# Kernel tuning notes

Hardware: AMD Instinct MI355X
Metric: run time of the kernel (lower is better)

## Reference

```python
import jax, jax.numpy as jnp
import numpy as np

B, NIMG, NTXT, D, H, MLP = 2, 2048, 256, 1024, 16, 4096
DH = D // H
EPS = 1e-6

def _ln(x):
    mu = jnp.mean(x, axis=-1, keepdims=True)
    var = jnp.var(x, axis=-1, keepdims=True)
    return (x - mu) * jax.lax.rsqrt(var + EPS)

def _mod(x, shift, scale):
    return x * (1.0 + scale[:, None, :]) + shift[:, None, :]

def setup_inputs():
    key = jax.random.key(0)
    ks = jax.random.split(key, 40)
    def w(i, shape):
        return jax.random.normal(ks[i], shape, jnp.float32) * 0.02
    inp = {
        'img_tokens': jax.random.normal(ks[0], (B, NIMG, D), jnp.float32),
        'txt_tokens': jax.random.normal(ks[1], (B, NTXT, D), jnp.float32),
        'c': jax.random.normal(ks[2], (B, D), jnp.float32),
    }
    for i, n in enumerate(['q_img', 'k_img', 'v_img', 'q_txt', 'k_txt', 'v_txt', 'out_img', 'out_txt']):
        inp[n + '_w'] = w(3 + i, (D, D))
        inp[n + '_b'] = w(11 + i, (D,))
    inp['mlp_img_w1'] = w(19, (MLP, D)); inp['mlp_img_b1'] = w(20, (MLP,))
    inp['mlp_img_w2'] = w(21, (D, MLP)); inp['mlp_img_b2'] = w(22, (D,))
    inp['mlp_txt_w1'] = w(23, (MLP, D)); inp['mlp_txt_b1'] = w(24, (MLP,))
    inp['mlp_txt_w2'] = w(25, (D, MLP)); inp['mlp_txt_b2'] = w(26, (D,))
    inp['adaln_img_w'] = w(27, (6 * D, D)); inp['adaln_img_b'] = w(28, (6 * D,))
    inp['adaln_txt_w'] = w(29, (6 * D, D)); inp['adaln_txt_b'] = w(30, (6 * D,))
    return inp

def reference(img_tokens, txt_tokens, c,
              q_img_w, q_img_b, k_img_w, k_img_b, v_img_w, v_img_b,
              q_txt_w, q_txt_b, k_txt_w, k_txt_b, v_txt_w, v_txt_b,
              out_img_w, out_img_b, out_txt_w, out_txt_b,
              mlp_img_w1, mlp_img_b1, mlp_img_w2, mlp_img_b2,
              mlp_txt_w1, mlp_txt_b1, mlp_txt_w2, mlp_txt_b2,
              adaln_img_w, adaln_img_b, adaln_txt_w, adaln_txt_b):
    lin = lambda x, w, b: x @ w.T + b
    mod_i = lin(jax.nn.silu(c), adaln_img_w, adaln_img_b)
    mod_t = lin(jax.nn.silu(c), adaln_txt_w, adaln_txt_b)
    sh_a_i, sc_a_i, g_a_i, sh_m_i, sc_m_i, g_m_i = jnp.split(mod_i, 6, axis=-1)
    sh_a_t, sc_a_t, g_a_t, sh_m_t, sc_m_t, g_m_t = jnp.split(mod_t, 6, axis=-1)
    img_n = _mod(_ln(img_tokens), sh_a_i, sc_a_i)
    txt_n = _mod(_ln(txt_tokens), sh_a_t, sc_a_t)
    heads = lambda x: x.reshape(x.shape[0], x.shape[1], H, DH)  # (B, N, H, DH)
    q_i = heads(lin(img_n, q_img_w, q_img_b))
    k_i = heads(lin(img_n, k_img_w, k_img_b))
    v_i = heads(lin(img_n, v_img_w, v_img_b))
    q_t = heads(lin(txt_n, q_txt_w, q_txt_b))
    k_t = heads(lin(txt_n, k_txt_w, k_txt_b))
    v_t = heads(lin(txt_n, v_txt_w, v_txt_b))
    # joint KV: each query attends over img+txt keys
    k_j = jnp.concatenate([k_i, k_t], axis=1)  # (B, NIMG+NTXT, H, DH)
    v_j = jnp.concatenate([v_i, v_t], axis=1)
    scale = DH ** -0.5
    def attend(q):
        s = jnp.einsum('bqhd,bkhd->bhqk', q, k_j) * scale
        a = jax.nn.softmax(s, axis=-1)
        o = jnp.einsum('bhqk,bkhd->bqhd', a, v_j)
        return o.reshape(o.shape[0], o.shape[1], D)
    a_img = lin(attend(q_i), out_img_w, out_img_b)
    a_txt = lin(attend(q_t), out_txt_w, out_txt_b)
    img = img_tokens + g_a_i[:, None, :] * a_img
    txt = txt_tokens + g_a_t[:, None, :] * a_txt
    mlp = lambda x, w1, b1, w2, b2: lin(jax.nn.gelu(lin(x, w1, b1), approximate=True), w2, b2)
    img = img + g_m_i[:, None, :] * mlp(_mod(_ln(img), sh_m_i, sc_m_i), mlp_img_w1, mlp_img_b1, mlp_img_w2, mlp_img_b2)
    txt = txt + g_m_t[:, None, :] * mlp(_mod(_ln(txt), sh_m_t, sc_m_t), mlp_txt_w1, mlp_txt_b1, mlp_txt_w2, mlp_txt_b2)
    return (img, txt)
```

## Files before the change

kernel.cpp:

```cpp
#include <hip/hip_runtime.h>
#include <hip/hip_bf16.h>

typedef __bf16 bf16_t;
typedef __bf16 bf16x8 __attribute__((ext_vector_type(8)));
typedef float f32x4 __attribute__((ext_vector_type(4)));

#define DEV static __device__ __forceinline__

#define QSCALE 0.18033688011112042f

DEV float gelu_tanh(float x){
    float x3 = x*x*x;
    return 0.5f*x*(1.0f + tanhf(0.79788456080286535588f*(x + 0.044715f*x3)));
}

DEV void gload16(const void* g, void* l){
    __builtin_amdgcn_global_load_lds((const __attribute__((address_space(1))) void*)g,
                                     (__attribute__((address_space(3))) void*)l, 16, 0, 0);
}

__global__ __launch_bounds__(256) void convert_pack(
    const float* qiw, const float* kiw, const float* viw,
    const float* qtw, const float* ktw, const float* vtw,
    const float* oiw, const float* otw,
    const float* m1iw, const float* m1tw, const float* m2iw, const float* m2tw,
    const float* qib, const float* kib, const float* vib,
    const float* qtb, const float* ktb, const float* vtb,
    bf16_t* wqkvI, bf16_t* wqkvT, bf16_t* woI, bf16_t* woT,
    bf16_t* wm1I, bf16_t* wm1T, bf16_t* wm2I, bf16_t* wm2T,
    float* qkvbI, float* qkvbT)
{
    const int MB = 1048576, MB4 = 4194304;
    int seg = blockIdx.y;
    const float* src = nullptr; bf16_t* dst = nullptr; float* dstf = nullptr; int n = 0;
    switch (seg){
        case 0:  src=qiw;  dst=wqkvI;        n=MB;   break;
        case 1:  src=kiw;  dst=wqkvI+MB;     n=MB;   break;
        case 2:  src=viw;  dst=wqkvI+2*MB;   n=MB;   break;
        case 3:  src=qtw;  dst=wqkvT;        n=MB;   break;
        case 4:  src=ktw;  dst=wqkvT+MB;     n=MB;   break;
        case 5:  src=vtw;  dst=wqkvT+2*MB;   n=MB;   break;
        case 6:  src=oiw;  dst=woI;          n=MB;   break;
        case 7:  src=otw;  dst=woT;          n=MB;   break;
        case 8:  src=m1iw; dst=wm1I;         n=MB4;  break;
        case 9:  src=m1tw; dst=wm1T;         n=MB4;  break;
        case 10: src=m2iw; dst=wm2I;         n=MB4;  break;
        case 11: src=m2tw; dst=wm2T;         n=MB4;  break;
        case 12: src=qib;  dstf=qkvbI;       n=1024; break;
        case 13: src=kib;  dstf=qkvbI+1024;  n=1024; break;
        case 14: src=vib;  dstf=qkvbI+2048;  n=1024; break;
        case 15: src=qtb;  dstf=qkvbT;       n=1024; break;
        case 16: src=ktb;  dstf=qkvbT+1024;  n=1024; break;
        case 17: src=vtb;  dstf=qkvbT+2048;  n=1024; break;
    }
    float scl = (seg==0 || seg==3 || seg==12 || seg==15) ? QSCALE : 1.0f;
    int n4 = n >> 2;
    for (int i = blockIdx.x*blockDim.x + threadIdx.x; i < n4; i += gridDim.x*blockDim.x){
        float4 v = ((const float4*)src)[i];
        v.x *= scl; v.y *= scl; v.z *= scl; v.w *= scl;
        if (dst){
            union { bf16_t b[4]; uint2 q; } o;
            o.b[0] = (bf16_t)v.x; o.b[1] = (bf16_t)v.y;
            o.b[2] = (bf16_t)v.z; o.b[3] = (bf16_t)v.w;
            ((uint2*)dst)[i] = o.q;
        } else {
            ((float4*)dstf)[i] = v;
        }
    }
}

__global__ __launch_bounds__(256) void adaln_kernel(
    const float* __restrict__ cvec,
    const float* __restrict__ wI, const float* __restrict__ bI,
    const float* __restrict__ wT, const float* __restrict__ bT,
    float* __restrict__ modI, float* __restrict__ modT)
{
    int oid0 = blockIdx.x * 16;
    int s    = oid0 / 12288;
    int rem  = oid0 - s*12288;
    int b    = rem / 6144;
    int col0 = rem - b*6144;
    const float* W  = s ? wT : wI;
    const float* Bv = s ? bT : bI;
    float* out = (s ? modT : modI) + b*6144;
    int lane = threadIdx.x & 63, w = threadIdx.x >> 6;
    float sc[16];
#pragma unroll
    for (int j = 0; j < 16; j++){
        float cv = cvec[b*1024 + lane + 64*j];
        sc[j] = cv / (1.0f + __expf(-cv));
    }
#pragma unroll
    for (int i = 0; i < 4; i++){
        int col = col0 + w*4 + i;
        const float* wr = W + (size_t)col*1024;
        float acc = 0.f;
#pragma unroll
        for (int j = 0; j < 16; j++) acc += sc[j]*wr[lane + 64*j];
        for (int d = 32; d; d >>= 1) acc += __shfl_down(acc, d);
        if (lane == 0) out[col] = acc + Bv[col];
    }
}

__global__ __launch_bounds__(256) void ln_mod_kernel(
    const float* __restrict__ xa, const float* __restrict__ xb,
    const float* __restrict__ moda, const float* __restrict__ modb,
    bf16_t* __restrict__ outa, bf16_t* __restrict__ outb,
    int rowsA, int nbA, int nbB, int shOff, int scOff)
{
    int row = blockIdx.x;
    const float* x; const float* mod; bf16_t* out;
    if (row < rowsA){
        int b = row / nbA;
        x = xa + (size_t)row*1024; mod = moda + b*6144; out = outa + (size_t)row*1024;
    } else {
        int r2 = row - rowsA; int b = r2 / nbB;
        x = xb + (size_t)r2*1024; mod = modb + b*6144; out = outb + (size_t)r2*1024;
    }
    int t = threadIdx.x;
    float4 v = ((const float4*)x)[t];
    float s  = v.x+v.y+v.z+v.w;
    float ss = v.x*v.x + v.y*v.y + v.z*v.z + v.w*v.w;
    for (int d = 32; d; d >>= 1){ s += __shfl_down(s, d); ss += __shfl_down(ss, d); }
    __shared__ float rs_[4], rss_[4];
    int wv = t >> 6;
    if ((t & 63) == 0){ rs_[wv] = s; rss_[wv] = ss; }
    __syncthreads();
    s  = rs_[0]+rs_[1]+rs_[2]+rs_[3];
    ss = rss_[0]+rss_[1]+rss_[2]+rss_[3];
    float mu   = s * (1.0f/1024.0f);
    float var  = ss * (1.0f/1024.0f) - mu*mu;
    float rstd = rsqrtf(var + 1e-6f);
    int c = t*4;
    float vv[4] = {v.x, v.y, v.z, v.w};
    union { bf16_t b4[4]; uint2 q; } ov;
#pragma unroll
    for (int i = 0; i < 4; i++){
        float scv = mod[scOff + c + i], shv = mod[shOff + c + i];
        ov.b4[i] = (bf16_t)(((vv[i]-mu)*rstd)*(1.0f+scv) + shv);
    }
    *(uint2*)(out + c) = ov.q;
}

template<int EPI>
__global__ __launch_bounds__(256) void gemm128(
    const bf16_t* __restrict__ A0, const bf16_t* __restrict__ A1,
    const bf16_t* __restrict__ W0, const bf16_t* __restrict__ W1,
    const float* __restrict__ bias0, const float* __restrict__ bias1,
    bf16_t* __restrict__ ob0, bf16_t* __restrict__ ob1,
    float* __restrict__ of0, float* __restrict__ of1,
    const float* __restrict__ res0, const float* __restrict__ res1,
    const float* __restrict__ mod0, const float* __restrict__ mod1,
    int gateOff, int rpb0, int rpb1, int MI, int N, int K)
{
    __shared__ bf16_t lsA[128*32];
    __shared__ bf16_t lsB[128*32];
    const int tid  = threadIdx.x;
    const int lane = tid & 63;
    const int w64  = tid & 192;
    const int wid  = tid >> 6;
    const int wm = wid & 1, wn = wid >> 1;
    const int m16 = lane & 15, quad = lane >> 4;
    const int bx = blockIdx.x, by = blockIdx.y;
    const int strm = (by >= MI) ? 1 : 0;
    const bf16_t* A = strm ? A1 : A0;
    const bf16_t* W = strm ? W1 : W0;
    const int rowBase = (strm ? by - MI : by) * 128;

    const bf16_t* Ab = A + (size_t)rowBase*K;
    const bf16_t* Wb = W + (size_t)(bx*128)*K;
    const int arow = tid >> 2, ach = (tid & 3) << 3;

    f32x4 acc[4][4];
#pragma unroll
    for (int mt = 0; mt < 4; mt++)
#pragma unroll
        for (int nt = 0; nt < 4; nt++) acc[mt][nt] = (f32x4){0.f,0.f,0.f,0.f};

    for (int kt = 0; kt < K; kt += 32){
        __syncthreads();
#pragma unroll
        for (int j = 0; j < 2; j++){
            int row = j*64 + arow;
            gload16(Ab + (size_t)row*K + kt + ach, lsA + (j*256 + w64)*8);
            gload16(Wb + (size_t)row*K + kt + ach, lsB + (j*256 + w64)*8);
        }
        __syncthreads();
        bf16x8 af[4], bf_[4];
#pragma unroll
        for (int mt = 0; mt < 4; mt++) af[mt]  = *(const bf16x8*)&lsA[(wm*64 + mt*16 + m16)*32 + quad*8];
#pragma unroll
        for (int nt = 0; nt < 4; nt++) bf_[nt] = *(const bf16x8*)&lsB[(wn*64 + nt*16 + m16)*32 + quad*8];
#pragma unroll
        for (int mt = 0; mt < 4; mt++)
#pragma unroll
            for (int nt = 0; nt < 4; nt++)
                acc[mt][nt] = __builtin_amdgcn_mfma_f32_16x16x32_bf16(af[mt], bf_[nt], acc[mt][nt], 0, 0, 0);
    }
    const float* bias = strm ? bias1 : bias0;
    bf16_t* ob = strm ? ob1 : ob0;
    float*  of = strm ? of1 : of0;
    const float* res = strm ? res1 : res0;
    const float* mod = strm ? mod1 : mod0;
    const int rpb = strm ? rpb1 : rpb0;
#pragma unroll
    for (int mt = 0; mt < 4; mt++){
#pragma unroll
        for (int nt = 0; nt < 4; nt++){
#pragma unroll
            for (int r = 0; r < 4; r++){
                int row = rowBase + wm*64 + mt*16 + quad*4 + r;
                int col = bx*128 + wn*64 + nt*16 + m16;
                float v = acc[mt][nt][r] + bias[col];
                if (EPI == 0){
                    ob[(size_t)row*N + col] = (bf16_t)v;
                } else if (EPI == 1){
                    int b = (row >= rpb) ? 1 : 0;
                    float g = mod[b*6144 + gateOff + col];
                    of[(size_t)row*N + col] = res[(size_t)row*N + col] + g*v;
                } else {
                    ob[(size_t)row*N + col] = (bf16_t)gelu_tanh(v);
                }
            }
        }
    }
}

template<int EPI>
__global__ __launch_bounds__(256) void gemm64(
    const bf16_t* __restrict__ A0, const bf16_t* __restrict__ A1,
    const bf16_t* __restrict__ W0, const bf16_t* __restrict__ W1,
    const float* __restrict__ bias0, const float* __restrict__ bias1,
    bf16_t* __restrict__ ob0, bf16_t* __restrict__ ob1,
    float* __restrict__ of0, float* __restrict__ of1,
    const float* __restrict__ res0, const float* __restrict__ res1,
    const float* __restrict__ mod0, const float* __restrict__ mod1,
    int gateOff, int rpb0, int rpb1, int MI, int N, int K)
{
    __shared__ bf16_t lsA[64*32];
    __shared__ bf16_t lsB[128*32];
    const int tid  = threadIdx.x;
    const int lane = tid & 63;
    const int w64  = tid & 192;
    const int wid  = tid >> 6;
    const int wm = wid & 1, wn = wid >> 1;
    const int m16 = lane & 15, quad = lane >> 4;
    const int bx = blockIdx.x, by = blockIdx.y;
    const int strm = (by >= MI) ? 1 : 0;
    const bf16_t* A = strm ? A1 : A0;
    const bf16_t* W = strm ? W1 : W0;
    const int rowBase = (strm ? by - MI : by) * 64;

    const bf16_t* Ab = A + (size_t)rowBase*K;
    const bf16_t* Wb = W + (size_t)(bx*128)*K;
    const int arow = tid >> 2, ach = (tid & 3) << 3;

    f32x4 acc[2][4];
#pragma unroll
    for (int mt = 0; mt < 2; mt++)
#pragma unroll
        for (int nt = 0; nt < 4; nt++) acc[mt][nt] = (f32x4){0.f,0.f,0.f,0.f};

    for (int kt = 0; kt < K; kt += 32){
        __syncthreads();
        gload16(Ab + (size_t)arow*K + kt + ach, lsA + w64*8);
#pragma unroll
        for (int j = 0; j < 2; j++){
            int row = j*64 + arow;
            gload16(Wb + (size_t)row*K + kt + ach, lsB + (j*256 + w64)*8);
        }
        __syncthreads();
        bf16x8 af[2], bf_[4];
#pragma unroll
        for (int mt = 0; mt < 2; mt++) af[mt]  = *(const bf16x8*)&lsA[(wm*32 + mt*16 + m16)*32 + quad*8];
#pragma unroll
        for (int nt = 0; nt < 4; nt++) bf_[nt] = *(const bf16x8*)&lsB[(wn*64 + nt*16 + m16)*32 + quad*8];
#pragma unroll
        for (int mt = 0; mt < 2; mt++)
#pragma unroll
            for (int nt = 0; nt < 4; nt++)
                acc[mt][nt] = __builtin_amdgcn_mfma_f32_16x16x32_bf16(af[mt], bf_[nt], acc[mt][nt], 0, 0, 0);
    }
    const float* bias = strm ? bias1 : bias0;
    bf16_t* ob = strm ? ob1 : ob0;
    float*  of = strm ? of1 : of0;
    const float* res = strm ? res1 : res0;
    const float* mod = strm ? mod1 : mod0;
    const int rpb = strm ? rpb1 : rpb0;
#pragma unroll
    for (int mt = 0; mt < 2; mt++){
#pragma unroll
        for (int nt = 0; nt < 4; nt++){
#pragma unroll
            for (int r = 0; r < 4; r++){
                int row = rowBase + wm*32 + mt*16 + quad*4 + r;
                int col = bx*128 + wn*64 + nt*16 + m16;
                float v = acc[mt][nt][r] + bias[col];
                if (EPI == 0){
                    ob[(size_t)row*N + col] = (bf16_t)v;
                } else if (EPI == 1){
                    int b = (row >= rpb) ? 1 : 0;
                    float g = mod[b*6144 + gateOff + col];
                    of[(size_t)row*N + col] = res[(size_t)row*N + col] + g*v;
                } else {
                    ob[(size_t)row*N + col] = (bf16_t)gelu_tanh(v);
                }
            }
        }
    }
}

__global__ __launch_bounds__(256) void vt_kernel(
    const bf16_t* __restrict__ qkvI, const bf16_t* __restrict__ qkvT,
    bf16_t* __restrict__ vt)
{
    int blk = blockIdx.x;
    int kt = blk % 36; int bh = blk / 36; int h = bh & 15; int b = bh >> 4;
    __shared__ bf16_t tile[64][72];
    int t = threadIdx.x;
    int krow = t >> 3;
    int cg   = (t & 7) * 8;
#pragma unroll
    for (int i = 0; i < 2; i++){
        int key = kt*64 + krow + i*32;
        const bf16_t* src = (key < 2048)
            ? qkvI + ((size_t)(b*2048 + key))*3072 + 2048 + h*64 + cg
            : qkvT + ((size_t)(b*256 + key - 2048))*3072 + 2048 + h*64 + cg;
        *(uint4*)&tile[krow + i*32][cg] = *(const uint4*)src;
    }
    __syncthreads();
#pragma unroll
    for (int i = 0; i < 2; i++){
        int idx = t + i*256;
        int dh = idx >> 3; int kg = (idx & 7)*8;
        union { bf16_t b8[8]; uint4 q; } o;
#pragma unroll
        for (int j = 0; j < 8; j++) o.b8[j] = tile[kg + j][dh];
        size_t off = ((size_t)((b*16 + h)*64 + dh))*2304 + kt*64 + kg;
        *(uint4*)&vt[off] = o.q;
    }
}

__global__ __launch_bounds__(256) void attn_kernel(
    const bf16_t* __restrict__ qkvI, const bf16_t* __restrict__ qkvT,
    const bf16_t* __restrict__ vt,
    float* __restrict__ opart, float* __restrict__ lpart)
{
    __shared__ bf16_t klds0[64*32], klds1[64*32];
    __shared__ bf16_t vlds0[64*32], vlds1[64*32];
    __shared__ bf16_t plds[4][32*72];
    const int qc = blockIdx.x;
    const int bh = blockIdx.y;
    const int ks = blockIdx.z;
    const int h = bh & 15, b = bh >> 4;
    const int t = threadIdx.x;
    const int w = t >> 6, lane = t & 63;
    const int m16 = lane & 15, quad = lane >> 4;
    const int isImg = (qc < 16);
    const int q0 = (isImg ? qc : qc - 16) * 128 + w*32;
    const int qj = isImg ? q0 : 2048 + q0;

    const bf16_t* qkvQ = isImg ? qkvI + (size_t)(b*2048 + q0)*3072
                               : qkvT + (size_t)(b*256  + q0)*3072;
    bf16x8 aq[2][2];
#pragma unroll
    for (int m = 0; m < 2; m++)
#pragma unroll
        for (int kc = 0; kc < 2; kc++)
            aq[m][kc] = *(const bf16x8*)(qkvQ + (size_t)(m*16 + m16)*3072 + h*64 + kc*32 + quad*8);

    f32x4 o[2][4], lacc[2];
#pragma unroll
    for (int m = 0; m < 2; m++){
        lacc[m] = (f32x4){0.f,0.f,0.f,0.f};
#pragma unroll
        for (int nt = 0; nt < 4; nt++) o[m][nt] = (f32x4){0.f,0.f,0.f,0.f};
    }
    bf16x8 ones;
#pragma unroll
    for (int i = 0; i < 8; i++) ones[i] = (bf16_t)1.0f;

    const bf16_t* vtb = vt + (size_t)(bh*64)*2304;
    const int rloc = lane >> 2;
    const int cc   = (lane & 3) << 3;
    bf16_t* pw = plds[w];

    for (int kt = ks*768; kt < ks*768 + 768; kt += 64){
        {
            int key = kt + w*16 + rloc;
            const bf16_t* kg = (key < 2048)
                ? qkvI + (size_t)(b*2048 + key)*3072 + 1024 + h*64
                : qkvT + (size_t)(b*256 + key - 2048)*3072 + 1024 + h*64;
            int dh = w*16 + rloc;
            const bf16_t* vg = vtb + (size_t)dh*2304 + kt;
            __syncthreads();
            gload16(kg + cc,      klds0 + w*512);
            gload16(kg + 32 + cc, klds1 + w*512);
            gload16(vg + cc,      vlds0 + w*512);
            gload16(vg + 32 + cc, vlds1 + w*512);
            __syncthreads();
        }
        f32x4 s[2][4];
#pragma unroll
        for (int m = 0; m < 2; m++)
#pragma unroll
            for (int c = 0; c < 4; c++) s[m][c] = (f32x4){0.f,0.f,0.f,0.f};
#pragma unroll
        for (int kc = 0; kc < 2; kc++){
            const bf16_t* kl = kc ? klds1 : klds0;
            bf16x8 kf[4];
#pragma unroll
            for (int c = 0; c < 4; c++) kf[c] = *(const bf16x8*)&kl[(c*16 + m16)*32 + quad*8];
#pragma unroll
            for (int m = 0; m < 2; m++)
#pragma unroll
                for (int c = 0; c < 4; c++)
                    s[m][c] = __builtin_amdgcn_mfma_f32_16x16x32_bf16(aq[m][kc], kf[c], s[m][c], 0, 0, 0);
        }
#pragma unroll
        for (int m = 0; m < 2; m++){
#pragma unroll
            for (int r = 0; r < 4; r++){
                int row = m*16 + quad*4 + r;
#pragma unroll
                for (int c = 0; c < 4; c++)
                    pw[row*72 + c*16 + m16] = (bf16_t)exp2f(s[m][c][r]);
            }
        }
        asm volatile("s_waitcnt lgkmcnt(0)" ::: "memory");
#pragma unroll
        for (int kc = 0; kc < 2; kc++){
            const bf16_t* vl = kc ? vlds1 : vlds0;
            bf16x8 pf0 = *(const bf16x8*)&pw[(m16)*72 + kc*32 + quad*8];
            bf16x8 pf1 = *(const bf16x8*)&pw[(16 + m16)*72 + kc*32 + quad*8];
            lacc[0] = __builtin_amdgcn_mfma_f32_16x16x32_bf16(pf0, ones, lacc[0], 0, 0, 0);
            lacc[1] = __builtin_amdgcn_mfma_f32_16x16x32_bf16(pf1, ones, lacc[1], 0, 0, 0);
#pragma unroll
            for (int nt = 0; nt < 4; nt++){
                bf16x8 vf = *(const bf16x8*)&vl[(nt*16 + m16)*32 + quad*8];
                o[0][nt] = __builtin_amdgcn_mfma_f32_16x16x32_bf16(pf0, vf, o[0][nt], 0, 0, 0);
                o[1][nt] = __builtin_amdgcn_mfma_f32_16x16x32_bf16(pf1, vf, o[1][nt], 0, 0, 0);
            }
        }
    }
    float* ob = opart + ((size_t)(ks*32 + bh)*2304 + qj)*64;
    float* lb = lpart + (size_t)(ks*32 + bh)*2304 + qj;
#pragma unroll
    for (int m = 0; m < 2; m++){
#pragma unroll
        for (int r = 0; r < 4; r++){
            int row = m*16 + quad*4 + r;
#pragma unroll
            for (int nt = 0; nt < 4; nt++)
                ob[(size_t)row*64 + nt*16 + m16] = o[m][nt][r];
            if (m16 == 0) lb[row] = lacc[m][r];
        }
    }
}

__global__ __launch_bounds__(256) void attn_combine(
    const float* __restrict__ opart, const float* __restrict__ lpart,
    bf16_t* __restrict__ attnI, bf16_t* __restrict__ attnT)
{
    const int gid = blockIdx.x*256 + threadIdx.x;
    const int row = gid >> 4;
    const int dq  = (gid & 15) << 2;
    float l = lpart[row] + lpart[73728 + row] + lpart[147456 + row];
    const float* p = opart + (size_t)row*64 + dq;
    float4 s0 = *(const float4*)(p);
    float4 s1 = *(const float4*)(p + 4718592);
    float4 s2 = *(const float4*)(p + 9437184);
    float inv = 1.0f / l;
    union { bf16_t b4[4]; uint2 q; } ov;
    ov.b4[0] = (bf16_t)((s0.x + s1.x + s2.x) * inv);
    ov.b4[1] = (bf16_t)((s0.y + s1.y + s2.y) * inv);
    ov.b4[2] = (bf16_t)((s0.z + s1.z + s2.z) * inv);
    ov.b4[3] = (bf16_t)((s0.w + s1.w + s2.w) * inv);
    int bh = row / 2304;
    int qj = row - bh*2304;
    int b = bh >> 4, h = bh & 15;
    bf16_t* dst = (qj < 2048)
        ? attnI + ((size_t)(b*2048 + qj)*1024 + h*64 + dq)
        : attnT + ((size_t)(b*256 + qj - 2048)*1024 + h*64 + dq);
    *(uint2*)dst = ov.q;
}

extern "C" void kernel_launch(void* const* d_in, const int* in_sizes, int n_in,
                              void* d_out, int out_size, void* d_ws, size_t ws_size,
                              hipStream_t stream)
{
    const float* img = (const float*)d_in[0];
    const float* txt = (const float*)d_in[1];
    const float* cv  = (const float*)d_in[2];
    const float* qiw = (const float*)d_in[3];   const float* qib = (const float*)d_in[4];
    const float* kiw = (const float*)d_in[5];   const float* kib = (const float*)d_in[6];
    const float* viw = (const float*)d_in[7];   const float* vib = (const float*)d_in[8];
    const float* qtw = (const float*)d_in[9];   const float* qtb = (const float*)d_in[10];
    const float* ktw = (const float*)d_in[11];  const float* ktb = (const float*)d_in[12];
    const float* vtw = (const float*)d_in[13];  const float* vtb = (const float*)d_in[14];
    const float* oiw = (const float*)d_in[15];  const float* oib = (const float*)d_in[16];
    const float* otw = (const float*)d_in[17];  const float* otb = (const float*)d_in[18];
    const float* m1iw = (const float*)d_in[19]; const float* m1ib = (const float*)d_in[20];
    const float* m2iw = (const float*)d_in[21]; const float* m2ib = (const float*)d_in[22];
    const float* m1tw = (const float*)d_in[23]; const float* m1tb = (const float*)d_in[24];
    const float* m2tw = (const float*)d_in[25]; const float* m2tb = (const float*)d_in[26];
    const float* adiw = (const float*)d_in[27]; const float* adib = (const float*)d_in[28];
    const float* adtw = (const float*)d_in[29]; const float* adtb = (const float*)d_in[30];
    float* out = (float*)d_out;

    char* ws = (char*)d_ws;
    size_t off = 0;
    auto alloc = [&](size_t bytes)->char*{
        char* p = ws + off; off += (bytes + 255) & ~(size_t)255; return p;
    };
    bf16_t* wqkvI = (bf16_t*)alloc(3145728u*2);
    bf16_t* wqkvT = (bf16_t*)alloc(3145728u*2);
    bf16_t* woI   = (bf16_t*)alloc(1048576u*2);
    bf16_t* woT   = (bf16_t*)alloc(1048576u*2);
    bf16_t* wm1I  = (bf16_t*)alloc(4194304u*2);
    bf16_t* wm1T  = (bf16_t*)alloc(4194304u*2);
    bf16_t* wm2I  = (bf16_t*)alloc(4194304u*2);
    bf16_t* wm2T  = (bf16_t*)alloc(4194304u*2);
    float*  qkvbI = (float*)alloc(3072u*4);
    float*  qkvbT = (float*)alloc(3072u*4);
    float*  modI  = (float*)alloc(12288u*4);
    float*  modT  = (float*)alloc(12288u*4);
    bf16_t* xnI   = (bf16_t*)alloc(4194304u*2);
    bf16_t* xnT   = (bf16_t*)alloc(524288u*2);
    bf16_t* qkvI  = (bf16_t*)alloc(12582912u*2);
    bf16_t* qkvT  = (bf16_t*)alloc(1572864u*2);
    bf16_t* vtb_  = (bf16_t*)alloc(4718592u*2);
    bf16_t* attnI = (bf16_t*)alloc(4194304u*2);
    bf16_t* attnT = (bf16_t*)alloc(524288u*2);
    float*  hI    = (float*)alloc(4194304u*4);
    float*  hT    = (float*)alloc(524288u*4);
    bf16_t* xn2I  = (bf16_t*)alloc(4194304u*2);
    bf16_t* xn2T  = (bf16_t*)alloc(524288u*2);
    bf16_t* mhI   = (bf16_t*)alloc(16777216u*2);
    bf16_t* mhT   = (bf16_t*)alloc(2097152u*2);
    float*  opart = (float*)alloc(14155776u*4);
    float*  lpart = (float*)alloc(221184u*4);
    (void)ws_size; (void)in_sizes; (void)n_in; (void)out_size;

    convert_pack<<<dim3(256,18,1), 256, 0, stream>>>(
        qiw,kiw,viw,qtw,ktw,vtw,oiw,otw,m1iw,m1tw,m2iw,m2tw,
        qib,kib,vib,qtb,ktb,vtb,
        wqkvI,wqkvT,woI,woT,wm1I,wm1T,wm2I,wm2T,qkvbI,qkvbT);

    adaln_kernel<<<1536, 256, 0, stream>>>(cv, adiw, adib, adtw, adtb, modI, modT);

    ln_mod_kernel<<<4608, 256, 0, stream>>>(img, txt, modI, modT, xnI, xnT,
                                            4096, 2048, 256, 0, 1024);

    gemm128<0><<<dim3(24,36), 256, 0, stream>>>(xnI, xnT, wqkvI, wqkvT,
        qkvbI, qkvbT, qkvI, qkvT, nullptr, nullptr, nullptr, nullptr,
        nullptr, nullptr, 0, 0, 0, 32, 3072, 1024);

    vt_kernel<<<1152, 256, 0, stream>>>(qkvI, qkvT, vtb_);
    attn_kernel<<<dim3(18,32,3), 256, 0, stream>>>(qkvI, qkvT, vtb_, opart, lpart);
    attn_combine<<<4608, 256, 0, stream>>>(opart, lpart, attnI, attnT);

    gemm64<1><<<dim3(8,72), 256, 0, stream>>>(attnI, attnT, woI, woT,
        oib, otb, nullptr, nullptr, hI, hT, img, txt, modI, modT,
        2048, 2048, 256, 64, 1024, 1024);

    ln_mod_kernel<<<4608, 256, 0, stream>>>(hI, hT, modI, modT, xn2I, xn2T,
                                            4096, 2048, 256, 3072, 4096);

    gemm128<2><<<dim3(32,36), 256, 0, stream>>>(xn2I, xn2T, wm1I, wm1T,
        m1ib, m1tb, mhI, mhT, nullptr, nullptr, nullptr, nullptr,
        nullptr, nullptr, 0, 0, 0, 32, 4096, 1024);

    gemm64<1><<<dim3(8,72), 256, 0, stream>>>(mhI, mhT, wm2I, wm2T,
        m2ib, m2tb, nullptr, nullptr, out, out + 4194304, hI, hT, modI, modT,
        5120, 2048, 256, 64, 1024, 4096);
}
```

Measured before the change: 645.2 us.

## Replace 64-row N=1024 GEMMs with split-K 128-tile GEMM plus combine kernel

The out-projection and MLP down-projection GEMMs move from a 64x128 tile kernel to the 128x128 tile kernel with a two-way split over K. Each split writes fp32 partial sums, and a new elementwise kernel then adds the partials, bias, gate and residual. This trades the lower per-block data reuse of the smaller tile for larger tiles while keeping a similar block count (8x36x2). The cost is extra fp32 partial traffic and one more launch per GEMM. The adaLN kernel also switches to float4 vector loads.

```diff
diff --git a/kernel.cpp b/kernel.cpp
--- a/kernel.cpp
+++ b/kernel.cpp
@@ -84,11 +84,14 @@
     const float* Bv = s ? bT : bI;
     float* out = (s ? modT : modI) + b*6144;
     int lane = threadIdx.x & 63, w = threadIdx.x >> 6;
-    float sc[16];
-#pragma unroll
-    for (int j = 0; j < 16; j++){
-        float cv = cvec[b*1024 + lane + 64*j];
-        sc[j] = cv / (1.0f + __expf(-cv));
+    float4 sc[4];
+#pragma unroll
+    for (int j = 0; j < 4; j++){
+        float4 cv = ((const float4*)(cvec + b*1024))[lane + 64*j];
+        sc[j].x = cv.x / (1.0f + __expf(-cv.x));
+        sc[j].y = cv.y / (1.0f + __expf(-cv.y));
+        sc[j].z = cv.z / (1.0f + __expf(-cv.z));
+        sc[j].w = cv.w / (1.0f + __expf(-cv.w));
     }
 #pragma unroll
     for (int i = 0; i < 4; i++){
@@ -96,7 +99,10 @@
         const float* wr = W + (size_t)col*1024;
         float acc = 0.f;
 #pragma unroll
-        for (int j = 0; j < 16; j++) acc += sc[j]*wr[lane + 64*j];
+        for (int j = 0; j < 4; j++){
+            float4 w4 = ((const float4*)wr)[lane + 64*j];
+            acc += sc[j].x*w4.x + sc[j].y*w4.y + sc[j].z*w4.z + sc[j].w*w4.w;
+        }
         for (int d = 32; d; d >>= 1) acc += __shfl_down(acc, d);
         if (lane == 0) out[col] = acc + Bv[col];
     }
@@ -149,9 +155,7 @@
     const float* __restrict__ bias0, const float* __restrict__ bias1,
     bf16_t* __restrict__ ob0, bf16_t* __restrict__ ob1,
     float* __restrict__ of0, float* __restrict__ of1,
-    const float* __restrict__ res0, const float* __restrict__ res1,
-    const float* __restrict__ mod0, const float* __restrict__ mod1,
-    int gateOff, int rpb0, int rpb1, int MI, int N, int K)
+    int MI, int N, int K, int Ksplit)
 {
     __shared__ bf16_t lsA[128*32];
     __shared__ bf16_t lsB[128*32];
@@ -166,6 +170,8 @@
     const bf16_t* A = strm ? A1 : A0;
     const bf16_t* W = strm ? W1 : W0;
     const int rowBase = (strm ? by - MI : by) * 128;
+    const int kBeg = blockIdx.z * Ksplit;
+    const int kEnd = kBeg + Ksplit;
 
     const bf16_t* Ab = A + (size_t)rowBase*K;
     const bf16_t* Wb = W + (size_t)(bx*128)*K;
@@ -177,7 +183,7 @@
 #pragma unroll
         for (int nt = 0; nt < 4; nt++) acc[mt][nt] = (f32x4){0.f,0.f,0.f,0.f};
 
-    for (int kt = 0; kt < K; kt += 32){
+    for (int kt = kBeg; kt < kEnd; kt += 32){
         __syncthreads();
 #pragma unroll
         for (int j = 0; j < 2; j++){
@@ -199,115 +205,56 @@
     }
     const float* bias = strm ? bias1 : bias0;
     bf16_t* ob = strm ? ob1 : ob0;
-    float*  of = strm ? of1 : of0;
-    const float* res = strm ? res1 : res0;
-    const float* mod = strm ? mod1 : mod0;
-    const int rpb = strm ? rpb1 : rpb0;
+    float* ofp = blockIdx.z ? of1 : of0;
 #pragma unroll
     for (int mt = 0; mt < 4; mt++){
 #pragma unroll
         for (int nt = 0; nt < 4; nt++){
 #pragma unroll
             for (int r = 0; r < 4; r++){
-                int row = rowBase + wm*64 + mt*16 + quad*4 + r;
+                int lrow = wm*64 + mt*16 + quad*4 + r;
                 int col = bx*128 + wn*64 + nt*16 + m16;
-                float v = acc[mt][nt][r] + bias[col];
                 if (EPI == 0){
-                    ob[(size_t)row*N + col] = (bf16_t)v;
-                } else if (EPI == 1){
-                    int b = (row >= rpb) ? 1 : 0;
-                    float g = mod[b*6144 + gateOff + col];
-                    of[(size_t)row*N + col] = res[(size_t)row*N + col] + g*v;
+                    ob[(size_t)(rowBase + lrow)*N + col] = (bf16_t)(acc[mt][nt][r] + bias[col]);
+                } else if (EPI == 2){
+                    ob[(size_t)(rowBase + lrow)*N + col] = (bf16_t)gelu_tanh(acc[mt][nt][r] + bias[col]);
                 } else {
-                    ob[(size_t)row*N + col] = (bf16_t)gelu_tanh(v);
+                    int jrow = by*128 + lrow;
+                    ofp[(size_t)jrow*N + col] = acc[mt][nt][r];
                 }
             }
         }
     }
 }
 
-template<int EPI>
-__global__ __launch_bounds__(256) void gemm64(
-    const bf16_t* __restrict__ A0, const bf16_t* __restrict__ A1,
-    const bf16_t* __restrict__ W0, const bf16_t* __restrict__ W1,
+__global__ __launch_bounds__(256) void combine2(
+    const float* __restrict__ p0, const float* __restrict__ p1,
     const float* __restrict__ bias0, const float* __restrict__ bias1,
-    bf16_t* __restrict__ ob0, bf16_t* __restrict__ ob1,
-    float* __restrict__ of0, float* __restrict__ of1,
     const float* __restrict__ res0, const float* __restrict__ res1,
     const float* __restrict__ mod0, const float* __restrict__ mod1,
-    int gateOff, int rpb0, int rpb1, int MI, int N, int K)
-{
-    __shared__ bf16_t lsA[64*32];
-    __shared__ bf16_t lsB[128*32];
-    const int tid  = threadIdx.x;
-    const int lane = tid & 63;
-    const int w64  = tid & 192;
-    const int wid  = tid >> 6;
-    const int wm = wid & 1, wn = wid >> 1;
-    const int m16 = lane & 15, quad = lane >> 4;
-    const int bx = blockIdx.x, by = blockIdx.y;
-    const int strm = (by >= MI) ? 1 : 0;
-    const bf16_t* A = strm ? A1 : A0;
-    const bf16_t* W = strm ? W1 : W0;
-    const int rowBase = (strm ? by - MI : by) * 64;
-
-    const bf16_t* Ab = A + (size_t)rowBase*K;
-    const bf16_t* Wb = W + (size_t)(bx*128)*K;
-    const int arow = tid >> 2, ach = (tid & 3) << 3;
-
-    f32x4 acc[2][4];
-#pragma unroll
-    for (int mt = 0; mt < 2; mt++)
-#pragma unroll
-        for (int nt = 0; nt < 4; nt++) acc[mt][nt] = (f32x4){0.f,0.f,0.f,0.f};
-
-    for (int kt = 0; kt < K; kt += 32){
-        __syncthreads();
-        gload16(Ab + (size_t)arow*K + kt + ach, lsA + w64*8);
-#pragma unroll
-        for (int j = 0; j < 2; j++){
-            int row = j*64 + arow;
-            gload16(Wb + (size_t)row*K + kt + ach, lsB + (j*256 + w64)*8);
-        }
-        __syncthreads();
-        bf16x8 af[2], bf_[4];
-#pragma unroll
-        for (int mt = 0; mt < 2; mt++) af[mt]  = *(const bf16x8*)&lsA[(wm*32 + mt*16 + m16)*32 + quad*8];
-#pragma unroll
-        for (int nt = 0; nt < 4; nt++) bf_[nt] = *(const bf16x8*)&lsB[(wn*64 + nt*16 + m16)*32 + quad*8];
-#pragma unroll
-        for (int mt = 0; mt < 2; mt++)
-#pragma unroll
-            for (int nt = 0; nt < 4; nt++)
-                acc[mt][nt] = __builtin_amdgcn_mfma_f32_16x16x32_bf16(af[mt], bf_[nt], acc[mt][nt], 0, 0, 0);
-    }
-    const float* bias = strm ? bias1 : bias0;
-    bf16_t* ob = strm ? ob1 : ob0;
-    float*  of = strm ? of1 : of0;
-    const float* res = strm ? res1 : res0;
-    const float* mod = strm ? mod1 : mod0;
-    const int rpb = strm ? rpb1 : rpb0;
-#pragma unroll
-    for (int mt = 0; mt < 2; mt++){
-#pragma unroll
-        for (int nt = 0; nt < 4; nt++){
-#pragma unroll
-            for (int r = 0; r < 4; r++){
-                int row = rowBase + wm*32 + mt*16 + quad*4 + r;
-                int col = bx*128 + wn*64 + nt*16 + m16;
-                float v = acc[mt][nt][r] + bias[col];
-                if (EPI == 0){
-                    ob[(size_t)row*N + col] = (bf16_t)v;
-                } else if (EPI == 1){
-                    int b = (row >= rpb) ? 1 : 0;
-                    float g = mod[b*6144 + gateOff + col];
-                    of[(size_t)row*N + col] = res[(size_t)row*N + col] + g*v;
-                } else {
-                    ob[(size_t)row*N + col] = (bf16_t)gelu_tanh(v);
-                }
-            }
-        }
-    }
+    float* __restrict__ dst0, float* __restrict__ dst1, int gateOff)
+{
+    int gid = blockIdx.x*256 + threadIdx.x;
+    int row = gid >> 8;
+    int col = (gid & 255) << 2;
+    float4 a  = *(const float4*)(p0 + (size_t)row*1024 + col);
+    float4 bq = *(const float4*)(p1 + (size_t)row*1024 + col);
+    int strm = row >= 4096;
+    int lr = strm ? row - 4096 : row;
+    int bb = lr / (strm ? 256 : 2048);
+    const float* bias = (strm ? bias1 : bias0) + col;
+    const float* res  = (strm ? res1 : res0) + (size_t)lr*1024 + col;
+    const float* mod  = (strm ? mod1 : mod0) + bb*6144 + gateOff + col;
+    float* dst = (strm ? dst1 : dst0) + (size_t)lr*1024 + col;
+    float4 bs = *(const float4*)bias;
+    float4 g  = *(const float4*)mod;
+    float4 rv = *(const float4*)res;
+    float4 o;
+    o.x = rv.x + g.x*(a.x + bq.x + bs.x);
+    o.y = rv.y + g.y*(a.y + bq.y + bs.y);
+    o.z = rv.z + g.z*(a.z + bq.z + bs.z);
+    o.w = rv.w + g.w*(a.w + bq.w + bs.w);
+    *(float4*)dst = o;
 }
 
 __global__ __launch_bounds__(256) void vt_kernel(
@@ -540,6 +487,8 @@
     bf16_t* mhT   = (bf16_t*)alloc(2097152u*2);
     float*  opart = (float*)alloc(14155776u*4);
     float*  lpart = (float*)alloc(221184u*4);
+    float*  pS0   = (float*)alloc(4718592u*4);
+    float*  pS1   = (float*)alloc(4718592u*4);
     (void)ws_size; (void)in_sizes; (void)n_in; (void)out_size;
 
     convert_pack<<<dim3(256,18,1), 256, 0, stream>>>(
@@ -553,25 +502,25 @@
                                             4096, 2048, 256, 0, 1024);
 
     gemm128<0><<<dim3(24,36), 256, 0, stream>>>(xnI, xnT, wqkvI, wqkvT,
-        qkvbI, qkvbT, qkvI, qkvT, nullptr, nullptr, nullptr, nullptr,
-        nullptr, nullptr, 0, 0, 0, 32, 3072, 1024);
+        qkvbI, qkvbT, qkvI, qkvT, nullptr, nullptr, 32, 3072, 1024, 1024);
 
     vt_kernel<<<1152, 256, 0, stream>>>(qkvI, qkvT, vtb_);
     attn_kernel<<<dim3(18,32,3), 256, 0, stream>>>(qkvI, qkvT, vtb_, opart, lpart);
     attn_combine<<<4608, 256, 0, stream>>>(opart, lpart, attnI, attnT);
 
-    gemm64<1><<<dim3(8,72), 256, 0, stream>>>(attnI, attnT, woI, woT,
-        oib, otb, nullptr, nullptr, hI, hT, img, txt, modI, modT,
-        2048, 2048, 256, 64, 1024, 1024);
+    gemm128<3><<<dim3(8,36,2), 256, 0, stream>>>(attnI, attnT, woI, woT,
+        nullptr, nullptr, nullptr, nullptr, pS0, pS1, 32, 1024, 1024, 512);
+    combine2<<<4608, 256, 0, stream>>>(pS0, pS1, oib, otb, img, txt,
+        modI, modT, hI, hT, 2048);
 
     ln_mod_kernel<<<4608, 256, 0, stream>>>(hI, hT, modI, modT, xn2I, xn2T,
                                             4096, 2048, 256, 3072, 4096);
 
     gemm128<2><<<dim3(32,36), 256, 0, stream>>>(xn2I, xn2T, wm1I, wm1T,
-        m1ib, m1tb, mhI, mhT, nullptr, nullptr, nullptr, nullptr,
-        nullptr, nullptr, 0, 0, 0, 32, 4096, 1024);
-
-    gemm64<1><<<dim3(8,72), 256, 0, stream>>>(mhI, mhT, wm2I, wm2T,
-        m2ib, m2tb, nullptr, nullptr, out, out + 4194304, hI, hT, modI, modT,
-        5120, 2048, 256, 64, 1024, 4096);
-}
+        m1ib, m1tb, mhI, mhT, nullptr, nullptr, 32, 4096, 1024, 1024);
+
+    gemm128<3><<<dim3(8,36,2), 256, 0, stream>>>(mhI, mhT, wm2I, wm2T,
+        nullptr, nullptr, nullptr, nullptr, pS0, pS1, 32, 1024, 4096, 2048);
+    combine2<<<4608, 256, 0, stream>>>(pS0, pS1, m2ib, m2tb, hI, hT,
+        modI, modT, out, out + 4194304, 5120);
+}
```

Measured after the change: 637.0 us. No clear change (-1.3%).
